# Performance work log

Hardware: AMD Instinct MI355X
Metric: run time of the kernel (lower is better)

## Reference

```python
import jax, jax.numpy as jnp
import numpy as np

B, C, L, E = 32, 3, 512, 512


def setup_inputs() -> dict:
    key = jax.random.key(0)
    ks = jax.random.split(key, 13)
    bnd = float(np.sqrt(6.0 / (2.0 * E)))  # xavier-uniform-like bound
    uni = lambda k, shp: jax.random.uniform(k, shp, jnp.float32, -bnd, bnd)
    return {
        "A0": jax.random.normal(ks[0], (B, C, L, L), jnp.float32),
        "x0": jax.random.normal(ks[1], (B, C, L, E), jnp.float32),
        "u0": jax.random.normal(ks[2], (B, C, E), jnp.float32),
        "t0": jax.random.normal(ks[3], (B, E), jnp.float32),
        "t1": jax.random.normal(ks[4], (B, E), jnp.float32),
        "Q_weight": uni(ks[5], (C, E, E)),
        "Q_bias": jnp.zeros((C, E), jnp.float32),
        "V_weight": uni(ks[6], (C, E, E)),
        "V_bias": jnp.zeros((C, E), jnp.float32),
        "K_weight": uni(ks[7], (C, E, E)),
        "K_bias": jnp.zeros((C, E), jnp.float32),
        "T_weight": uni(ks[8], (C, E, E)),
        "T_bias": jnp.zeros((C, E), jnp.float32),
    }


def reference(A0, x0, u0, t0, t1,
              Q_weight, Q_bias, V_weight, V_bias,
              K_weight, K_bias, T_weight, T_bias):
    # Time embeddings: (B,E) @ (C,E,E) -> (B,C,E)
    T0 = jnp.einsum('be,cef->bcf', t0, T_weight)
    T1 = jnp.einsum('be,cef->bcf', t1, T_weight)

    # Original modulates weight columns: x @ (W * T) == (x @ W) * T (T broadcasts
    # over the input axis via unsqueeze(-2)); use the fused, equivalent form.
    Q = jnp.einsum('bce,cef->bcf', x0[:, :, -1, :], Q_weight) * T0 + Q_bias  # (B,C,E)
    K = jnp.einsum('bce,cef->bcf', u0, K_weight) * T1 + K_bias               # (B,C,E)
    V = jnp.einsum('bcle,cef->bclf', x0, V_weight) * T1[:, :, None, :] \
        + V_bias[None, :, None, :]                                           # (B,C,L,E)

    QKV = jax.nn.softmax(jnp.einsum('bce,bcle->bcl', Q * K, V), axis=-1)     # (B,C,L)

    # A1[:, :, i, :] = A0[:, :, i+1, :] - A0[:, :, 0, :] for i < L-1;
    # A1[:, :, L-1, :] = A1[:, :, L-2, :] + QKV  (= A0[-1] - A0[0] + QKV)
    rows = A0[:, :, 1:, :] - A0[:, :, :1, :]                                 # (B,C,L-1,L)
    last = rows[:, :, -1, :] + QKV                                           # (B,C,L)
    A1 = jnp.concatenate([rows, last[:, :, None, :]], axis=2)                # (B,C,L,L)

    x1 = jnp.einsum('bclm,bcme->bcle', A1, x0)                               # (B,C,L,E)
    x1 = jnp.diff(x1, axis=2, prepend=jnp.zeros_like(x1[:, :, :1, :]))

    num = jnp.sum(T0 * T1, axis=-1)                                          # (B,C)
    den = jnp.sqrt(jnp.sum(T0 * T0, axis=-1) + jnp.sum(T1 * T1, axis=-1))
    w = (num / den)[..., None]                                               # (B,C,1)

    u1 = u0 * (1.0 - w) + x1.mean(axis=-2) * w                               # (B,C,E)
    return (A1 - A0, x1 - x0, u1 - u0)
```

## Files before the change

### kernel.cpp

```cpp
#include <hip/hip_runtime.h>
#include <stdint.h>

#define BB 32
#define CC 3
#define LL 512
#define EE 512
#define NBC (BB*CC)

#define O2_OFF ((size_t)NBC*LL*LL)
#define O3_OFF (O2_OFF + (size_t)NBC*LL*EE)

#define WSB_QX    0
#define WSB_H     196608
#define WSB_W     442368
#define WSB_ADIFF ((size_t)512*1024)
#define ADIFF_BYTES ((size_t)NBC*LL*LL*2)
#define WS_FAST_NEED (WSB_ADIFF + ADIFF_BYTES)

#define NEC 16

typedef short bf16x8 __attribute__((ext_vector_type(8)));
typedef float f32x4  __attribute__((ext_vector_type(4)));
typedef unsigned short u16x8 __attribute__((ext_vector_type(8)));

__device__ __forceinline__ float wred_sum(float v){
#pragma unroll
  for (int m = 32; m >= 1; m >>= 1) v += __shfl_xor(v, m, 64);
  return v;
}
__device__ __forceinline__ float wred_max(float v){
#pragma unroll
  for (int m = 32; m >= 1; m >>= 1) v = fmaxf(v, __shfl_xor(v, m, 64));
  return v;
}
__device__ __forceinline__ void f4ma(float4& a, float s, const float4& b){
  a.x = fmaf(s, b.x, a.x); a.y = fmaf(s, b.y, a.y);
  a.z = fmaf(s, b.z, a.z); a.w = fmaf(s, b.w, a.w);
}
__device__ __forceinline__ float4 f4sub(const float4& a, const float4& b){
  return make_float4(a.x-b.x, a.y-b.y, a.z-b.z, a.w-b.w);
}
__device__ __forceinline__ unsigned short f2bf(float x){
  unsigned u = __float_as_uint(x);
  return (unsigned short)((u + 0x7FFFu + ((u >> 16) & 1u)) >> 16);
}
__device__ __forceinline__ float bf2f(unsigned short h){
  return __uint_as_float(((unsigned)h) << 16);
}
__device__ __forceinline__ void split1(float v, unsigned short& hi, unsigned short& lo){
  hi = f2bf(v);
  lo = f2bf(v - bf2f(hi));
}
__device__ __forceinline__ void st_nt_f4(float* p, float4 v){
  f32x4 w; w[0]=v.x; w[1]=v.y; w[2]=v.z; w[3]=v.w;
  __builtin_nontemporal_store(w, reinterpret_cast<f32x4*>(p));
}
__device__ __forceinline__ void st_nt_f(float* p, float v){
  __builtin_nontemporal_store(v, p);
}

__global__ __launch_bounds__(512) void conv2m(
    const float* __restrict__ A0, const float* __restrict__ x0,
    const float* __restrict__ u0,
    const float* __restrict__ t0, const float* __restrict__ t1,
    const float* __restrict__ Qw, const float* __restrict__ Kw,
    const float* __restrict__ Tw,
    char* __restrict__ adiff,
    float* __restrict__ P)
{
  const int bid = blockIdx.x;
  const int t = threadIdx.x;
  __shared__ float vb[4][4][32];

  if (bid < 768) {
    const int bc = bid >> 3, tile = bid & 7;
    const int r0 = tile*64;
    const size_t abase = (size_t)bc*LL*LL;
    char* ad = adiff + (size_t)bc*LL*LL*2;
    const int q4 = t & 127, rg = t >> 7;
    const int base = r0 + rg*16;
    float4 prev = *reinterpret_cast<const float4*>(A0 + abase + (size_t)base*LL + q4*4);
#pragma unroll 4
    for (int i = 0; i < 16; ++i) {
      int gr = base + i;
      float4 cur;
      if (gr + 1 < LL)
        cur = *reinterpret_cast<const float4*>(A0 + abase + (size_t)(gr+1)*LL + q4*4);
      else cur = prev;
      float4 d;
      if (gr < LL-1) d = f4sub(cur, prev);
      else           d = make_float4(0.f,0.f,0.f,0.f);
      if ((gr >> 2) == q4) {
        int e = gr & 3;
        d.x -= (e == 0) ? 1.0f : 0.0f;
        d.y -= (e == 1) ? 1.0f : 0.0f;
        d.z -= (e == 2) ? 1.0f : 0.0f;
        d.w -= (e == 3) ? 1.0f : 0.0f;
      }
      ushort4 pk;
      pk.x = f2bf(d.x); pk.y = f2bf(d.y); pk.z = f2bf(d.z); pk.w = f2bf(d.w);
      *reinterpret_cast<ushort4*>(ad + (size_t)gr*1024 + q4*8) = pk;
      prev = cur;
    }
  } else {
    const int idx = bid - 768;
    const int bg = idx & 7;
    const int rem = idx >> 3;
    const int c  = rem % 3;
    const int ec = rem / 3;
    const int b0 = bg*4;
    const int e0 = ec*32;
    const int f  = t;
    {
      int vec = f >> 7, j = (f >> 5) & 3, e = f & 31;
      int bb = b0 + j;
      float v;
      if      (vec == 0) v = t0[bb*EE + e0 + e];
      else if (vec == 1) v = t1[bb*EE + e0 + e];
      else if (vec == 2) v = x0[((size_t)(bb*CC + c)*LL + (LL-1))*EE + e0 + e];
      else               v = u0[(size_t)(bb*CC + c)*EE + e0 + e];
      vb[vec][j][e] = v;
    }
    __syncthreads();
    const float* twp = Tw + (size_t)c*EE*EE + (size_t)e0*EE + f;
    const float* qwp = Qw + (size_t)c*EE*EE + (size_t)e0*EE + f;
    const float* kwp = Kw + (size_t)c*EE*EE + (size_t)e0*EE + f;
    float aT0[4]={0,0,0,0}, aT1[4]={0,0,0,0}, aQ[4]={0,0,0,0}, aK[4]={0,0,0,0};
#pragma unroll 8
    for (int e = 0; e < 32; ++e) {
      float wt = twp[(size_t)e*EE];
      float wq = qwp[(size_t)e*EE];
      float wk = kwp[(size_t)e*EE];
#pragma unroll
      for (int j = 0; j < 4; ++j) {
        aT0[j] = fmaf(vb[0][j][e], wt, aT0[j]);
        aT1[j] = fmaf(vb[1][j][e], wt, aT1[j]);
        aQ[j]  = fmaf(vb[2][j][e], wq, aQ[j]);
        aK[j]  = fmaf(vb[3][j][e], wk, aK[j]);
      }
    }
#pragma unroll
    for (int j = 0; j < 4; ++j) {
      int cb = c*BB + b0 + j;
      P[(((size_t)0*NEC + ec)*96 + cb)*EE + f] = aT0[j];
      P[(((size_t)1*NEC + ec)*96 + cb)*EE + f] = aT1[j];
      P[(((size_t)2*NEC + ec)*96 + cb)*EE + f] = aQ[j];
      P[(((size_t)3*NEC + ec)*96 + cb)*EE + f] = aK[j];
    }
  }
}

__global__ __launch_bounds__(512) void k0c(
    const float* __restrict__ P,
    const float* __restrict__ Qb, const float* __restrict__ Kb,
    float* __restrict__ gtbuf, float* __restrict__ ws_w)
{
  const int bc = blockIdx.x;
  const int b = bc / CC, c = bc % CC;
  const int cb = c*BB + b;
  const int f = threadIdx.x;
  const int wid = f >> 6, lane = f & 63;
  __shared__ float red[8][3];
  float aT0=0.f, aT1=0.f, aQ=0.f, aK=0.f;
#pragma unroll
  for (int ec = 0; ec < NEC; ++ec) {
    aT0 += P[(((size_t)0*NEC + ec)*96 + cb)*EE + f];
    aT1 += P[(((size_t)1*NEC + ec)*96 + cb)*EE + f];
    aQ  += P[(((size_t)2*NEC + ec)*96 + cb)*EE + f];
    aK  += P[(((size_t)3*NEC + ec)*96 + cb)*EE + f];
  }
  float Qv = aQ*aT0 + Qb[c*EE + f];
  float Kv = aK*aT1 + Kb[c*EE + f];
  gtbuf[(size_t)cb*EE + f] = Qv*Kv*aT1;
  float pn = wred_sum(aT0*aT1);
  float p0 = wred_sum(aT0*aT0);
  float p1 = wred_sum(aT1*aT1);
  if (lane == 0) { red[wid][0]=pn; red[wid][1]=p0; red[wid][2]=p1; }
  __syncthreads();
  if (f == 0) {
    float sn=0.f, s0=0.f, s1=0.f;
    for (int i=0;i<8;++i){ sn+=red[i][0]; s0+=red[i][1]; s1+=red[i][2]; }
    ws_w[bc] = sn / sqrtf(s0 + s1);
  }
}

__global__ __launch_bounds__(256) void k1_h(
    const float* __restrict__ Vw, const float* __restrict__ gtbuf,
    float* __restrict__ ws_h)
{
  const int nt = blockIdx.x;
  const int c  = blockIdx.y;
  const int n0 = nt*128;
  const int t = threadIdx.x, lane = t & 63, w = t >> 6;
  __shared__ __align__(16) char AgtH[32*1024];
  __shared__ __align__(16) char AgtL[32*1024];
  __shared__ __align__(16) char BvH[128*128];
  __shared__ __align__(16) char BvL[128*128];
  {
    int row = t >> 3, sl = t & 7;
    const float* src = gtbuf + ((size_t)(c*BB + row))*EE + sl*64;
#pragma unroll
    for (int c3 = 0; c3 < 8; ++c3) {
      float4 a = *reinterpret_cast<const float4*>(src + c3*8);
      float4 b = *reinterpret_cast<const float4*>(src + c3*8 + 4);
      ushort4 h0,h1,l0,l1;
      split1(a.x,h0.x,l0.x); split1(a.y,h0.y,l0.y); split1(a.z,h0.z,l0.z); split1(a.w,h0.w,l0.w);
      split1(b.x,h1.x,l1.x); split1(b.y,h1.y,l1.y); split1(b.z,h1.z,l1.z); split1(b.w,h1.w,l1.w);
      int off = row*1024 + sl*128 + ((c3 ^ (row & 7)) << 4);
      *reinterpret_cast<ushort4*>(AgtH + off)     = h0;
      *reinterpret_cast<ushort4*>(AgtH + off + 8) = h1;
      *reinterpret_cast<ushort4*>(AgtL + off)     = l0;
      *reinterpret_cast<ushort4*>(AgtL + off + 8) = l1;
    }
  }
  f32x4 acc[2][2];
#pragma unroll
  for (int mi=0; mi<2; ++mi)
#pragma unroll
    for (int ni=0; ni<2; ++ni) acc[mi][ni] = (f32x4){0.f,0.f,0.f,0.f};

  for (int kk = 0; kk < 8; ++kk) {
    __syncthreads();
    {
      int nl = t >> 1, half = t & 1;
      const float* src = Vw + (size_t)c*EE*EE + (size_t)(n0+nl)*EE + kk*64 + half*32;
#pragma unroll
      for (int q = 0; q < 4; ++q) {
        float4 a = *reinterpret_cast<const float4*>(src + q*8);
        float4 b = *reinterpret_cast<const float4*>(src + q*8 + 4);
        int c3 = half*4 + q;
        ushort4 h0,h1,l0,l1;
        split1(a.x,h0.x,l0.x); split1(a.y,h0.y,l0.y); split1(a.z,h0.z,l0.z); split1(a.w,h0.w,l0.w);
        split1(b.x,h1.x,l1.x); split1(b.y,h1.y,l1.y); split1(b.z,h1.z,l1.z); split1(b.w,h1.w,l1.w);
        int off = nl*128 + ((c3 ^ (nl & 7)) << 4);
        *reinterpret_cast<ushort4*>(BvH + off)     = h0;
        *reinterpret_cast<ushort4*>(BvH + off + 8) = h1;
        *reinterpret_cast<ushort4*>(BvL + off)     = l0;
        *reinterpret_cast<ushort4*>(BvL + off + 8) = l1;
      }
    }
    __syncthreads();
    bf16x8 afH[2][2], afL[2][2], bfH[2][2], bfL[2][2];
#pragma unroll
    for (int mi=0; mi<2; ++mi)
#pragma unroll
      for (int ks=0; ks<2; ++ks) {
        int row = mi*16 + (lane & 15);
        int c3 = ks*4 + (lane >> 4);
        int off = row*1024 + kk*128 + ((c3 ^ (row & 7)) << 4);
        afH[mi][ks] = *reinterpret_cast<const bf16x8*>(AgtH + off);
        afL[mi][ks] = *reinterpret_cast<const bf16x8*>(AgtL + off);
      }
#pragma unroll
    for (int ni=0; ni<2; ++ni)
#pragma unroll
      for (int ks=0; ks<2; ++ks) {
        int n = w*32 + ni*16 + (lane & 15);
        int c3 = ks*4 + (lane >> 4);
        int off = n*128 + ((c3 ^ (n & 7)) << 4);
        bfH[ni][ks] = *reinterpret_cast<const bf16x8*>(BvH + off);
        bfL[ni][ks] = *reinterpret_cast<const bf16x8*>(BvL + off);
      }
#pragma unroll
    for (int mi=0; mi<2; ++mi)
#pragma unroll
      for (int ni=0; ni<2; ++ni)
#pragma unroll
        for (int ks=0; ks<2; ++ks) {
          acc[mi][ni] = __builtin_amdgcn_mfma_f32_16x16x32_bf16(afH[mi][ks], bfH[ni][ks], acc[mi][ni], 0, 0, 0);
          acc[mi][ni] = __builtin_amdgcn_mfma_f32_16x16x32_bf16(afH[mi][ks], bfL[ni][ks], acc[mi][ni], 0, 0, 0);
          acc[mi][ni] = __builtin_amdgcn_mfma_f32_16x16x32_bf16(afL[mi][ks], bfH[ni][ks], acc[mi][ni], 0, 0, 0);
        }
  }
#pragma unroll
  for (int mi=0; mi<2; ++mi)
#pragma unroll
    for (int ni=0; ni<2; ++ni)
#pragma unroll
      for (int r=0; r<4; ++r) {
        int b = mi*16 + (lane >> 4)*4 + r;
        int e = n0 + w*32 + ni*16 + (lane & 15);
        ws_h[((size_t)(b*CC + c))*EE + e] = acc[mi][ni][r];
      }
}

__global__ __launch_bounds__(512) void k2f(
    const float* __restrict__ A0, const float* __restrict__ x0,
    const float* __restrict__ u0,
    const float* __restrict__ ws_h, const float* __restrict__ ws_w,
    float* __restrict__ out1, float* __restrict__ out2, float* __restrict__ out3)
{
  const int bc = blockIdx.x;
  const int tid = threadIdx.x, wid = tid >> 6, lane = tid & 63;
  __shared__ __align__(16) float hb[EE], sb[LL], a0r0[LL], a0r3[LL];
  __shared__ float red[8];
  __shared__ float partl[4][12][128];
  const size_t abase = (size_t)bc*LL*LL;
  const size_t xbase = (size_t)bc*LL*EE;
  hb[tid]   = ws_h[(size_t)bc*EE + tid];
  a0r0[tid] = A0[abase + tid];
  a0r3[tid] = A0[abase + (size_t)(LL-1)*LL + tid];
  __syncthreads();
  const float4 h0 = *reinterpret_cast<const float4*>(&hb[lane*8]);
  const float4 h1 = *reinterpret_cast<const float4*>(&hb[lane*8+4]);
  for (int l = wid; l < LL; l += 8) {
    const float4* xr = reinterpret_cast<const float4*>(x0 + xbase + (size_t)l*EE);
    float4 v0 = xr[lane*2], v1 = xr[lane*2+1];
    float acc = v0.x*h0.x + v0.y*h0.y + v0.z*h0.z + v0.w*h0.w
              + v1.x*h1.x + v1.y*h1.y + v1.z*h1.z + v1.w*h1.w;
    acc = wred_sum(acc);
    if (lane == 0) sb[l] = acc;
  }
  __syncthreads();
  float v = sb[tid];
  float mx = wred_max(v);
  if (lane == 0) red[wid] = mx;
  __syncthreads();
  mx = red[0];
#pragma unroll
  for (int i = 1; i < 8; ++i) mx = fmaxf(mx, red[i]);
  float ev = __expf(v - mx);
  float sm = wred_sum(ev);
  __syncthreads();
  if (lane == 0) red[wid] = sm;
  __syncthreads();
  float tot = 0.f;
#pragma unroll
  for (int i = 0; i < 8; ++i) tot += red[i];
  float qk = ev / tot;
  sb[tid] = qk;
  st_nt_f(out1 + abase + (size_t)(LL-1)*LL + tid, qk - a0r0[tid]);
  __syncthreads();
  const int mg = tid >> 7, cg = tid & 127;
  float4 aq = make_float4(0,0,0,0), a0s = make_float4(0,0,0,0), a3s = make_float4(0,0,0,0);
#pragma unroll 4
  for (int i = 0; i < 128; ++i) {
    int m = mg*128 + i;
    float4 xv = *reinterpret_cast<const float4*>(x0 + xbase + (size_t)m*EE + cg*4);
    float qm = sb[m], z0 = a0r0[m], z3 = a0r3[m];
    f4ma(aq, qm, xv); f4ma(a0s, z0, xv); f4ma(a3s, z3, xv);
  }
#pragma unroll
  for (int k = 0; k < 4; ++k) {
    partl[mg][0+k][cg] = (&aq.x)[k];
    partl[mg][4+k][cg] = (&a0s.x)[k];
    partl[mg][8+k][cg] = (&a3s.x)[k];
  }
  __syncthreads();
  if (mg == 0) {
    float wv = ws_w[bc];
    float4 uv  = *reinterpret_cast<const float4*>(u0 + (size_t)bc*EE + cg*4);
    float4 x51 = *reinterpret_cast<const float4*>(x0 + xbase + (size_t)(LL-1)*EE + cg*4);
    float4 qx4, o3;
#pragma unroll
    for (int k = 0; k < 4; ++k) {
      float q = 0.f, y0 = 0.f, y3 = 0.f;
#pragma unroll
      for (int g = 0; g < 4; ++g) {
        q  += partl[g][0+k][cg];
        y0 += partl[g][4+k][cg];
        y3 += partl[g][8+k][cg];
      }
      (&qx4.x)[k] = q;
      (&o3.x)[k] = wv * ((y3 - y0 + q) * (1.f/(float)LL) - (&uv.x)[k]);
    }
    st_nt_f4(out2 + xbase + (size_t)(LL-1)*EE + cg*4, f4sub(qx4, x51));
    st_nt_f4(out3 + (size_t)bc*EE + cg*4, o3);
  }
}

#define ASTR 80
__global__ __launch_bounds__(256) void k3_bf(
    const char* __restrict__ adiff, const float* __restrict__ x0,
    const float* __restrict__ A0,
    float* __restrict__ out1, float* __restrict__ out2)
{
  const int bc = blockIdx.y;
  const int rt = blockIdx.x >> 2, nt = blockIdx.x & 3;
  const int r0 = rt*128, n0b = nt*128;
  const int t = threadIdx.x;
  const int lane = t & 63, wid = t >> 6;
  const int wr = wid >> 1, wc = wid & 1;
  __shared__ __align__(16) char As[128*ASTR];
  __shared__ __align__(16) char Bs[128*ASTR];
  __shared__ __align__(16) float zr[LL];
  const char* ad = adiff + (size_t)bc*LL*LL*2;
  const size_t abase = (size_t)bc*LL*LL;
  const size_t xbase = (size_t)bc*LL*EE;
  zr[t]       = A0[abase + t];
  zr[t + 256] = A0[abase + t + 256];
  f32x4 acc[4][4];
#pragma unroll
  for (int mi=0; mi<4; ++mi)
#pragma unroll
    for (int ni=0; ni<4; ++ni) acc[mi][ni] = (f32x4){0.f,0.f,0.f,0.f};

  const int bkl = (t & 7) * 4;
  const int bn0 = (t >> 3) * 4;

  for (int k0 = 0; k0 < LL; k0 += 32) {
    __syncthreads();
#pragma unroll
    for (int i = 0; i < 2; ++i) {
      int idx = i*256 + t;
      int row = idx >> 2, c = idx & 3;
      int4 v = *reinterpret_cast<const int4*>(ad + (size_t)(r0+row)*1024 + k0*2 + c*16);
      *reinterpret_cast<int4*>(As + row*ASTR + c*16) = v;
    }
    {
      float xq[4][4];
#pragma unroll
      for (int i = 0; i < 4; ++i)
        *reinterpret_cast<float4*>(xq[i]) =
          *reinterpret_cast<const float4*>(x0 + xbase + (size_t)(k0+bkl+i)*EE + n0b + bn0);
#pragma unroll
      for (int j = 0; j < 4; ++j) {
        int n = bn0 + j;
        ushort4 pk;
        pk.x = f2bf(xq[0][j]); pk.y = f2bf(xq[1][j]);
        pk.z = f2bf(xq[2][j]); pk.w = f2bf(xq[3][j]);
        int kb = (bkl*2) ^ (((n >> 2) & 3) << 4);
        *reinterpret_cast<ushort4*>(Bs + n*ASTR + kb) = pk;
      }
    }
    __syncthreads();
    bf16x8 af[4], bfv[4];
#pragma unroll
    for (int mi=0; mi<4; ++mi) {
      int row = wr*64 + mi*16 + (lane & 15);
      af[mi] = *reinterpret_cast<const bf16x8*>(As + row*ASTR + ((lane>>4)*16));
    }
#pragma unroll
    for (int ni=0; ni<4; ++ni) {
      int n = wc*64 + ni*16 + (lane & 15);
      int kb = ((lane>>4)*16) ^ (((n >> 2) & 3) << 4);
      bfv[ni] = *reinterpret_cast<const bf16x8*>(Bs + n*ASTR + kb);
    }
#pragma unroll
    for (int mi=0; mi<4; ++mi)
#pragma unroll
      for (int ni=0; ni<4; ++ni)
        acc[mi][ni] = __builtin_amdgcn_mfma_f32_16x16x32_bf16(af[mi], bfv[ni], acc[mi][ni], 0, 0, 0);
    if (((k0 >> 5) & 3) == nt) {
      const int c4 = (t & 7) * 4;
      const int gcol0 = k0 + c4;
      const float4 zz = *reinterpret_cast<const float4*>(&zr[gcol0]);
#pragma unroll
      for (int rr = 0; rr < 4; ++rr) {
        int row = rr*32 + (t >> 3);
        int gr = r0 + row;
        if (gr < LL-1) {
          ushort4 ap = *reinterpret_cast<const ushort4*>(As + row*ASTR + c4*2);
          float4 o;
          o.x = bf2f(ap.x); o.y = bf2f(ap.y); o.z = bf2f(ap.z); o.w = bf2f(ap.w);
          int e = gr - gcol0;
          o.x += (e == 0) ? 1.0f : 0.0f;
          o.y += (e == 1) ? 1.0f : 0.0f;
          o.z += (e == 2) ? 1.0f : 0.0f;
          o.w += (e == 3) ? 1.0f : 0.0f;
          st_nt_f4(out1 + abase + (size_t)gr*LL + gcol0, f4sub(o, zz));
        }
      }
    }
  }
#pragma unroll
  for (int mi=0; mi<4; ++mi)
#pragma unroll
    for (int r=0; r<4; ++r) {
      int grow = r0 + wr*64 + mi*16 + (lane>>4)*4 + r;
      if (grow >= LL-1) continue;
      const size_t rowoff = xbase + (size_t)grow*EE;
#pragma unroll
      for (int ni=0; ni<4; ++ni) {
        int gcol = n0b + wc*64 + ni*16 + (lane & 15);
        st_nt_f(out2 + rowoff + gcol, acc[mi][ni][r]);
      }
    }
}

__global__ __launch_bounds__(512) void kA_fused(
    const float* __restrict__ A0, const float* __restrict__ x0,
    const float* __restrict__ u0,
    const float* __restrict__ t0, const float* __restrict__ t1,
    const float* __restrict__ Qw, const float* __restrict__ Qb,
    const float* __restrict__ Vw,
    const float* __restrict__ Kw, const float* __restrict__ Kb,
    const float* __restrict__ Tw,
    float* __restrict__ ws_qx, float* __restrict__ out1, float* __restrict__ out3)
{
  const int bc = blockIdx.x;
  const int b = bc / CC, c = bc % CC;
  const int tid = threadIdx.x;
  const int wid = tid >> 6, lane = tid & 63;
  __shared__ __align__(16) float t0v[EE], t1v[EE], xl[EE], uv[EE], gt[EE];
  __shared__ __align__(16) float hb[EE], sb[LL], a0r0[LL], a0r3[LL];
  __shared__ float red[3][8];
  __shared__ float wsh;
  const size_t abase = (size_t)bc*LL*LL;
  const size_t xbase = (size_t)bc*LL*EE;

  t0v[tid] = t0[b*EE + tid];
  t1v[tid] = t1[b*EE + tid];
  xl[tid]  = x0[xbase + (size_t)(LL-1)*EE + tid];
  uv[tid]  = u0[(size_t)bc*EE + tid];
  a0r0[tid] = A0[abase + tid];
  a0r3[tid] = A0[abase + (size_t)(LL-1)*LL + tid];
  __syncthreads();

  const int f = tid;
  const float* twp = Tw + (size_t)c*EE*EE + f;
  const float* qwp = Qw + (size_t)c*EE*EE + f;
  const float* kwp = Kw + (size_t)c*EE*EE + f;
  float aT0 = 0.f, aT1 = 0.f, aQ = 0.f, aK = 0.f;
  for (int e = 0; e < EE; ++e) {
    float wt = twp[(size_t)e*EE];
    aT0 = fmaf(t0v[e], wt, aT0);
    aT1 = fmaf(t1v[e], wt, aT1);
    aQ  = fmaf(xl[e],  qwp[(size_t)e*EE], aQ);
    aK  = fmaf(uv[e],  kwp[(size_t)e*EE], aK);
  }
  float Qv = aQ*aT0 + Qb[c*EE + f];
  float Kv = aK*aT1 + Kb[c*EE + f];
  gt[f] = Qv*Kv*aT1;

  float pn = wred_sum(aT0*aT1);
  float p0 = wred_sum(aT0*aT0);
  float p1 = wred_sum(aT1*aT1);
  if (lane == 0) { red[0][wid]=pn; red[1][wid]=p0; red[2][wid]=p1; }
  __syncthreads();
  if (tid == 0) {
    float sn=0.f, s0=0.f, s1=0.f;
    for (int i=0;i<8;++i){ sn+=red[0][i]; s0+=red[1][i]; s1+=red[2][i]; }
    wsh = sn / sqrtf(s0 + s1);
  }
  {
    const float4 g0 = *reinterpret_cast<const float4*>(&gt[lane*8]);
    const float4 g1 = *reinterpret_cast<const float4*>(&gt[lane*8+4]);
    for (int r = wid; r < EE; r += 8) {
      const float4* vr = reinterpret_cast<const float4*>(Vw + ((size_t)c*EE + r)*EE);
      float4 v0 = vr[lane*2], v1 = vr[lane*2+1];
      float acc = v0.x*g0.x + v0.y*g0.y + v0.z*g0.z + v0.w*g0.w
                + v1.x*g1.x + v1.y*g1.y + v1.z*g1.z + v1.w*g1.w;
      acc = wred_sum(acc);
      if (lane == 0) hb[r] = acc;
    }
  }
  __syncthreads();

  {
    const float4 h0 = *reinterpret_cast<const float4*>(&hb[lane*8]);
    const float4 h1 = *reinterpret_cast<const float4*>(&hb[lane*8+4]);
    for (int l = wid; l < LL; l += 8) {
      const float4* xr = reinterpret_cast<const float4*>(x0 + xbase + (size_t)l*EE);
      float4 v0 = xr[lane*2], v1 = xr[lane*2+1];
      float acc = v0.x*h0.x + v0.y*h0.y + v0.z*h0.z + v0.w*h0.w
                + v1.x*h1.x + v1.y*h1.y + v1.z*h1.z + v1.w*h1.w;
      acc = wred_sum(acc);
      if (lane == 0) sb[l] = acc;
    }
  }
  __syncthreads();

  float v = sb[tid];
  float mx = wred_max(v);
  if (lane == 0) red[0][wid] = mx;
  __syncthreads();
  mx = red[0][0];
#pragma unroll
  for (int i = 1; i < 8; ++i) mx = fmaxf(mx, red[0][i]);
  float ev = __expf(v - mx);
  float sm = wred_sum(ev);
  __syncthreads();
  if (lane == 0) red[0][wid] = sm;
  __syncthreads();
  float tot = 0.f;
#pragma unroll
  for (int i = 0; i < 8; ++i) tot += red[0][i];
  float qk = ev / tot;
  sb[tid] = qk;
  out1[abase + (size_t)(LL-1)*LL + tid] = qk - a0r0[tid];
  __syncthreads();

  float qx=0.f, y0=0.f, y3=0.f;
  for (int m = 0; m < LL; ++m) {
    float xm = x0[xbase + (size_t)m*EE + tid];
    qx = fmaf(sb[m],   xm, qx);
    y0 = fmaf(a0r0[m], xm, y0);
    y3 = fmaf(a0r3[m], xm, y3);
  }
  ws_qx[(size_t)bc*EE + tid] = qx;
  float mean = (y3 - y0 + qx) * (1.f/(float)LL);
  out3[(size_t)bc*EE + tid] = wsh * (mean - uv[tid]);
}

__global__ __launch_bounds__(256) void k3_mfma(
    const float* __restrict__ A0, const float* __restrict__ x0,
    const float* __restrict__ ws_qx,
    float* __restrict__ out1, float* __restrict__ out2)
{
  const int bc = blockIdx.y;
  const int rt = blockIdx.x >> 2, nt = blockIdx.x & 3;
  const int r0 = rt*128, n0b = nt*128;
  const int t = threadIdx.x;
  const int lane = t & 63, wid = t >> 6;
  const int wr = wid >> 1, wc = wid & 1;
  __shared__ __align__(16) char As[128*ASTR];
  __shared__ __align__(16) char Bs[128*ASTR];
  const size_t abase = (size_t)bc*LL*LL;
  const size_t xbase = (size_t)bc*LL*EE;
  f32x4 acc[4][4];
#pragma unroll
  for (int mi=0; mi<4; ++mi)
#pragma unroll
    for (int ni=0; ni<4; ++ni) acc[mi][ni] = (f32x4){0.f,0.f,0.f,0.f};
  const int bkl = (t & 7) * 4;
  const int bn0 = (t >> 3) * 4;
  for (int k0 = 0; k0 < LL; k0 += 32) {
    __syncthreads();
#pragma unroll
    for (int i = 0; i < 4; ++i) {
      int idx = i*256 + t;
      int row = idx >> 3, kq = idx & 7;
      int gr = r0 + row;
      int gr1 = (gr+1 > LL-1) ? (LL-1) : (gr+1);
      float4 va = *reinterpret_cast<const float4*>(A0 + abase + (size_t)gr *LL + k0 + kq*4);
      float4 vb = *reinterpret_cast<const float4*>(A0 + abase + (size_t)gr1*LL + k0 + kq*4);
      ushort4 pk;
      pk.x = f2bf(vb.x - va.x); pk.y = f2bf(vb.y - va.y);
      pk.z = f2bf(vb.z - va.z); pk.w = f2bf(vb.w - va.w);
      *reinterpret_cast<ushort4*>(As + row*ASTR + kq*8) = pk;
      if (nt == 0 && gr < LL-1) {
        float4 az = *reinterpret_cast<const float4*>(A0 + abase + k0 + kq*4);
        float4 o = make_float4(vb.x - az.x - va.x, vb.y - az.y - va.y,
                               vb.z - az.z - va.z, vb.w - az.w - va.w);
        *reinterpret_cast<float4*>(out1 + abase + (size_t)gr*LL + k0 + kq*4) = o;
      }
    }
    {
      float xq[4][4];
#pragma unroll
      for (int i = 0; i < 4; ++i)
        *reinterpret_cast<float4*>(xq[i]) =
          *reinterpret_cast<const float4*>(x0 + xbase + (size_t)(k0+bkl+i)*EE + n0b + bn0);
#pragma unroll
      for (int j = 0; j < 4; ++j) {
        int n = bn0 + j;
        ushort4 pk;
        pk.x = f2bf(xq[0][j]); pk.y = f2bf(xq[1][j]);
        pk.z = f2bf(xq[2][j]); pk.w = f2bf(xq[3][j]);
        int kb = (bkl*2) ^ (((n >> 2) & 3) << 4);
        *reinterpret_cast<ushort4*>(Bs + n*ASTR + kb) = pk;
      }
    }
    __syncthreads();
    bf16x8 af[4], bfv[4];
#pragma unroll
    for (int mi=0; mi<4; ++mi) {
      int row = wr*64 + mi*16 + (lane & 15);
      af[mi] = *reinterpret_cast<const bf16x8*>(As + row*ASTR + ((lane>>4)*16));
    }
#pragma unroll
    for (int ni=0; ni<4; ++ni) {
      int n = wc*64 + ni*16 + (lane & 15);
      int kb = ((lane>>4)*16) ^ (((n >> 2) & 3) << 4);
      bfv[ni] = *reinterpret_cast<const bf16x8*>(Bs + n*ASTR + kb);
    }
#pragma unroll
    for (int mi=0; mi<4; ++mi)
#pragma unroll
      for (int ni=0; ni<4; ++ni)
        acc[mi][ni] = __builtin_amdgcn_mfma_f32_16x16x32_bf16(af[mi], bfv[ni], acc[mi][ni], 0, 0, 0);
  }
#pragma unroll
  for (int mi=0; mi<4; ++mi)
#pragma unroll
    for (int r=0; r<4; ++r) {
      int grow = r0 + wr*64 + mi*16 + (lane>>4)*4 + r;
      const size_t rowoff = xbase + (size_t)grow*EE;
#pragma unroll
      for (int ni=0; ni<4; ++ni) {
        int gcol = n0b + wc*64 + ni*16 + (lane & 15);
        float xv = x0[rowoff + gcol];
        float val;
        if (grow == LL-1) val = ws_qx[(size_t)bc*EE + gcol] - xv;
        else              val = acc[mi][ni][r] - xv;
        out2[rowoff + gcol] = val;
      }
    }
}

extern "C" void kernel_launch(void* const* d_in, const int* in_sizes, int n_in,
                              void* d_out, int out_size, void* d_ws, size_t ws_size,
                              hipStream_t stream)
{
  const float* A0 = (const float*)d_in[0];
  const float* x0 = (const float*)d_in[1];
  const float* u0 = (const float*)d_in[2];
  const float* t0 = (const float*)d_in[3];
  const float* t1 = (const float*)d_in[4];
  const float* Qw = (const float*)d_in[5];
  const float* Qb = (const float*)d_in[6];
  const float* Vw = (const float*)d_in[7];
  const float* Kw = (const float*)d_in[9];
  const float* Kb = (const float*)d_in[10];
  const float* Tw = (const float*)d_in[11];

  char*  wsb    = (char*)d_ws;
  float* ws_qx  = (float*)(wsb + WSB_QX);
  float* ws_h   = (float*)(wsb + WSB_H);
  float* ws_w   = (float*)(wsb + WSB_W);

  float* out1 = (float*)d_out;
  float* out2 = out1 + O2_OFF;
  float* out3 = out1 + O3_OFF;
  float* gtbuf = out3;
  float* pscr  = out2;

  const bool fast = ws_size >= WS_FAST_NEED;

  if (fast) {
    char* adiff = wsb + WSB_ADIFF;
    conv2m<<<1152, 512, 0, stream>>>(A0, x0, u0, t0, t1, Qw, Kw, Tw,
                                     adiff, pscr);
    k0c<<<NBC, 512, 0, stream>>>(pscr, Qb, Kb, gtbuf, ws_w);
    k1_h<<<dim3(4, 3), 256, 0, stream>>>(Vw, gtbuf, ws_h);
    k2f<<<NBC, 512, 0, stream>>>(A0, x0, u0, ws_h, ws_w, out1, out2, out3);
    k3_bf<<<dim3(16, NBC), 256, 0, stream>>>(adiff, x0, A0, out1, out2);
  } else {
    kA_fused<<<NBC, 512, 0, stream>>>(A0, x0, u0, t0, t1, Qw, Qb, Vw, Kw, Kb, Tw,
                                      ws_qx, out1, out3);
    k3_mfma<<<dim3(16, NBC), 256, 0, stream>>>(A0, x0, ws_qx, out1, out2);
  }
}
```

Before: 230.8 us.

## Fuse softmax/last-row kernel into GEMM kernel as an extra block column

Merges the per-(b,c) softmax and last-row kernel into the bf16 MFMA GEMM kernel by adding a 17th block in the x-grid dimension that runs the former k2f work with 256 threads. This removes one kernel launch and lets that work overlap with the GEMM tiles. In exchange the fused blocks run with half the threads, so each one loops twice as long, and shared memory becomes one union buffer that every block allocates. The long-running extra blocks could become a tail that stretches the whole kernel.

```diff
diff --git a/kernel.cpp b/kernel.cpp
--- a/kernel.cpp
+++ b/kernel.cpp
@@ -284,109 +284,111 @@
       }
 }
 
-__global__ __launch_bounds__(512) void k2f(
-    const float* __restrict__ A0, const float* __restrict__ x0,
-    const float* __restrict__ u0,
+#define ASTR 80
+__global__ __launch_bounds__(256) void k3m(
+    const char* __restrict__ adiff, const float* __restrict__ x0,
+    const float* __restrict__ A0, const float* __restrict__ u0,
     const float* __restrict__ ws_h, const float* __restrict__ ws_w,
     float* __restrict__ out1, float* __restrict__ out2, float* __restrict__ out3)
 {
-  const int bc = blockIdx.x;
-  const int tid = threadIdx.x, wid = tid >> 6, lane = tid & 63;
-  __shared__ __align__(16) float hb[EE], sb[LL], a0r0[LL], a0r3[LL];
-  __shared__ float red[8];
-  __shared__ float partl[4][12][128];
+  const int bc = blockIdx.y;
+  const int t = threadIdx.x;
+  __shared__ __align__(16) char smem[22528];
   const size_t abase = (size_t)bc*LL*LL;
   const size_t xbase = (size_t)bc*LL*EE;
-  hb[tid]   = ws_h[(size_t)bc*EE + tid];
-  a0r0[tid] = A0[abase + tid];
-  a0r3[tid] = A0[abase + (size_t)(LL-1)*LL + tid];
-  __syncthreads();
-  const float4 h0 = *reinterpret_cast<const float4*>(&hb[lane*8]);
-  const float4 h1 = *reinterpret_cast<const float4*>(&hb[lane*8+4]);
-  for (int l = wid; l < LL; l += 8) {
-    const float4* xr = reinterpret_cast<const float4*>(x0 + xbase + (size_t)l*EE);
-    float4 v0 = xr[lane*2], v1 = xr[lane*2+1];
-    float acc = v0.x*h0.x + v0.y*h0.y + v0.z*h0.z + v0.w*h0.w
-              + v1.x*h1.x + v1.y*h1.y + v1.z*h1.z + v1.w*h1.w;
-    acc = wred_sum(acc);
-    if (lane == 0) sb[l] = acc;
-  }
-  __syncthreads();
-  float v = sb[tid];
-  float mx = wred_max(v);
-  if (lane == 0) red[wid] = mx;
-  __syncthreads();
-  mx = red[0];
-#pragma unroll
-  for (int i = 1; i < 8; ++i) mx = fmaxf(mx, red[i]);
-  float ev = __expf(v - mx);
-  float sm = wred_sum(ev);
-  __syncthreads();
-  if (lane == 0) red[wid] = sm;
-  __syncthreads();
-  float tot = 0.f;
-#pragma unroll
-  for (int i = 0; i < 8; ++i) tot += red[i];
-  float qk = ev / tot;
-  sb[tid] = qk;
-  st_nt_f(out1 + abase + (size_t)(LL-1)*LL + tid, qk - a0r0[tid]);
-  __syncthreads();
-  const int mg = tid >> 7, cg = tid & 127;
-  float4 aq = make_float4(0,0,0,0), a0s = make_float4(0,0,0,0), a3s = make_float4(0,0,0,0);
+  const int lane = t & 63, wid = t >> 6;
+
+  if (blockIdx.x == 16) {
+    float* hb   = (float*)(smem);
+    float* sbv  = (float*)(smem + 2048);
+    float* a0r0 = (float*)(smem + 4096);
+    float* a0r3 = (float*)(smem + 6144);
+    float* red  = (float*)(smem + 8192);
+    float (*partl)[12][128] = reinterpret_cast<float(*)[12][128]>(smem + 8320);
+    hb[t]       = ws_h[(size_t)bc*EE + t];
+    hb[t+256]   = ws_h[(size_t)bc*EE + t + 256];
+    a0r0[t]     = A0[abase + t];
+    a0r0[t+256] = A0[abase + t + 256];
+    a0r3[t]     = A0[abase + (size_t)(LL-1)*LL + t];
+    a0r3[t+256] = A0[abase + (size_t)(LL-1)*LL + t + 256];
+    __syncthreads();
+    const float4 h0 = *reinterpret_cast<const float4*>(&hb[lane*8]);
+    const float4 h1 = *reinterpret_cast<const float4*>(&hb[lane*8+4]);
+    for (int l = wid; l < LL; l += 4) {
+      const float4* xr = reinterpret_cast<const float4*>(x0 + xbase + (size_t)l*EE);
+      float4 v0 = xr[lane*2], v1 = xr[lane*2+1];
+      float acc = v0.x*h0.x + v0.y*h0.y + v0.z*h0.z + v0.w*h0.w
+                + v1.x*h1.x + v1.y*h1.y + v1.z*h1.z + v1.w*h1.w;
+      acc = wred_sum(acc);
+      if (lane == 0) sbv[l] = acc;
+    }
+    __syncthreads();
+    float v0 = sbv[t], v1 = sbv[t+256];
+    float mx = wred_max(fmaxf(v0, v1));
+    if (lane == 0) red[wid] = mx;
+    __syncthreads();
+    mx = red[0];
+#pragma unroll
+    for (int i = 1; i < 4; ++i) mx = fmaxf(mx, red[i]);
+    float ev0 = __expf(v0 - mx), ev1 = __expf(v1 - mx);
+    float sm = wred_sum(ev0 + ev1);
+    __syncthreads();
+    if (lane == 0) red[wid] = sm;
+    __syncthreads();
+    float tot = 0.f;
+#pragma unroll
+    for (int i = 0; i < 4; ++i) tot += red[i];
+    float qk0 = ev0 / tot, qk1 = ev1 / tot;
+    sbv[t] = qk0; sbv[t+256] = qk1;
+    st_nt_f(out1 + abase + (size_t)(LL-1)*LL + t,       qk0 - a0r0[t]);
+    st_nt_f(out1 + abase + (size_t)(LL-1)*LL + t + 256, qk1 - a0r0[t+256]);
+    __syncthreads();
+    const int mg = t >> 7, cg = t & 127;
+    float4 aq = make_float4(0,0,0,0), a0s = make_float4(0,0,0,0), a3s = make_float4(0,0,0,0);
 #pragma unroll 4
-  for (int i = 0; i < 128; ++i) {
-    int m = mg*128 + i;
-    float4 xv = *reinterpret_cast<const float4*>(x0 + xbase + (size_t)m*EE + cg*4);
-    float qm = sb[m], z0 = a0r0[m], z3 = a0r3[m];
-    f4ma(aq, qm, xv); f4ma(a0s, z0, xv); f4ma(a3s, z3, xv);
-  }
-#pragma unroll
-  for (int k = 0; k < 4; ++k) {
-    partl[mg][0+k][cg] = (&aq.x)[k];
-    partl[mg][4+k][cg] = (&a0s.x)[k];
-    partl[mg][8+k][cg] = (&a3s.x)[k];
-  }
-  __syncthreads();
-  if (mg == 0) {
-    float wv = ws_w[bc];
-    float4 uv  = *reinterpret_cast<const float4*>(u0 + (size_t)bc*EE + cg*4);
-    float4 x51 = *reinterpret_cast<const float4*>(x0 + xbase + (size_t)(LL-1)*EE + cg*4);
-    float4 qx4, o3;
+    for (int i = 0; i < 256; ++i) {
+      int m = mg*256 + i;
+      float4 xv = *reinterpret_cast<const float4*>(x0 + xbase + (size_t)m*EE + cg*4);
+      float qm = sbv[m], z0 = a0r0[m], z3 = a0r3[m];
+      f4ma(aq, qm, xv); f4ma(a0s, z0, xv); f4ma(a3s, z3, xv);
+    }
 #pragma unroll
     for (int k = 0; k < 4; ++k) {
-      float q = 0.f, y0 = 0.f, y3 = 0.f;
-#pragma unroll
-      for (int g = 0; g < 4; ++g) {
-        q  += partl[g][0+k][cg];
-        y0 += partl[g][4+k][cg];
-        y3 += partl[g][8+k][cg];
-      }
-      (&qx4.x)[k] = q;
-      (&o3.x)[k] = wv * ((y3 - y0 + q) * (1.f/(float)LL) - (&uv.x)[k]);
-    }
-    st_nt_f4(out2 + xbase + (size_t)(LL-1)*EE + cg*4, f4sub(qx4, x51));
-    st_nt_f4(out3 + (size_t)bc*EE + cg*4, o3);
-  }
-}
-
-#define ASTR 80
-__global__ __launch_bounds__(256) void k3_bf(
-    const char* __restrict__ adiff, const float* __restrict__ x0,
-    const float* __restrict__ A0,
-    float* __restrict__ out1, float* __restrict__ out2)
-{
-  const int bc = blockIdx.y;
+      partl[mg][0+k][cg] = (&aq.x)[k];
+      partl[mg][4+k][cg] = (&a0s.x)[k];
+      partl[mg][8+k][cg] = (&a3s.x)[k];
+    }
+    __syncthreads();
+    if (mg == 0) {
+      float wv = ws_w[bc];
+      float4 uv  = *reinterpret_cast<const float4*>(u0 + (size_t)bc*EE + cg*4);
+      float4 x51 = *reinterpret_cast<const float4*>(x0 + xbase + (size_t)(LL-1)*EE + cg*4);
+      float4 qx4, o3;
+#pragma unroll
+      for (int k = 0; k < 4; ++k) {
+        float q = 0.f, y0 = 0.f, y3 = 0.f;
+#pragma unroll
+        for (int g = 0; g < 2; ++g) {
+          q  += partl[g][0+k][cg];
+          y0 += partl[g][4+k][cg];
+          y3 += partl[g][8+k][cg];
+        }
+        (&qx4.x)[k] = q;
+        (&o3.x)[k] = wv * ((y3 - y0 + q) * (1.f/(float)LL) - (&uv.x)[k]);
+      }
+      st_nt_f4(out2 + xbase + (size_t)(LL-1)*EE + cg*4, f4sub(qx4, x51));
+      st_nt_f4(out3 + (size_t)bc*EE + cg*4, o3);
+    }
+    return;
+  }
+
   const int rt = blockIdx.x >> 2, nt = blockIdx.x & 3;
   const int r0 = rt*128, n0b = nt*128;
-  const int t = threadIdx.x;
-  const int lane = t & 63, wid = t >> 6;
   const int wr = wid >> 1, wc = wid & 1;
-  __shared__ __align__(16) char As[128*ASTR];
-  __shared__ __align__(16) char Bs[128*ASTR];
-  __shared__ __align__(16) float zr[LL];
+  char* As = smem;
+  char* Bs = smem + 128*ASTR;
+  float* zr = (float*)(smem + 2*128*ASTR);
   const char* ad = adiff + (size_t)bc*LL*LL*2;
-  const size_t abase = (size_t)bc*LL*LL;
-  const size_t xbase = (size_t)bc*LL*EE;
   zr[t]       = A0[abase + t];
   zr[t + 256] = A0[abase + t + 256];
   f32x4 acc[4][4];
@@ -724,8 +726,8 @@
                                      adiff, pscr);
     k0c<<<NBC, 512, 0, stream>>>(pscr, Qb, Kb, gtbuf, ws_w);
     k1_h<<<dim3(4, 3), 256, 0, stream>>>(Vw, gtbuf, ws_h);
-    k2f<<<NBC, 512, 0, stream>>>(A0, x0, u0, ws_h, ws_w, out1, out2, out3);
-    k3_bf<<<dim3(16, NBC), 256, 0, stream>>>(adiff, x0, A0, out1, out2);
+    k3m<<<dim3(17, NBC), 256, 0, stream>>>(adiff, x0, A0, u0, ws_h, ws_w,
+                                           out1, out2, out3);
   } else {
     kA_fused<<<NBC, 512, 0, stream>>>(A0, x0, u0, t0, t1, Qw, Qb, Vw, Kw, Kb, Tw,
                                       ws_qx, out1, out3);
```

After: 257.0 us. 1.11x slower.
